# Performance work log

Hardware: AMD Instinct MI355X
Metric: run time of the kernel (lower is better)

Reference implementation:

```python
import jax, jax.numpy as jnp
import numpy as np

EMBED_DIM = 1024
NUM_HEADS = 16
HEAD_DIM = EMBED_DIM // NUM_HEADS
SCALE = HEAD_DIM ** (-0.5)


def setup_inputs() -> dict:
    key = jax.random.key(0)
    ks = jax.random.split(key, 8)
    B, Nq, Nkv, C = 2, 2048, 2048, EMBED_DIM
    s = C ** (-0.5)
    return {
        "q": jax.random.normal(ks[0], (B, Nq, C), dtype=jnp.float32),
        "kv": jax.random.normal(ks[1], (B, Nkv, C), dtype=jnp.float32),
        "w_q": jax.random.normal(ks[2], (C, C), dtype=jnp.float32) * s,
        "b_q": jnp.zeros((C,), dtype=jnp.float32),
        "w_kv": jax.random.normal(ks[3], (C, 2 * C), dtype=jnp.float32) * s,
        "b_kv": jnp.zeros((2 * C,), dtype=jnp.float32),
        "w_out": jax.random.normal(ks[4], (C, C), dtype=jnp.float32) * s,
        "b_out": jnp.zeros((C,), dtype=jnp.float32),
    }


def reference(q, kv, w_q, b_q, w_kv, b_kv, w_out, b_out):
    B, Nq, C = q.shape
    _, Nkv, _ = kv.shape
    H, D = NUM_HEADS, HEAD_DIM

    # q projection: (B, Nq, C) -> (B, H, Nq, D)
    qp = (q @ w_q + b_q).reshape(B, Nq, H, D).transpose(0, 2, 1, 3)

    # kv projection: (B, Nkv, 2C) -> (2, B, H, Nkv, D); '(two h d)' layout
    kvp = (kv @ w_kv + b_kv).reshape(B, Nkv, 2, H, D).transpose(2, 0, 3, 1, 4)
    kp, vp = kvp[0], kvp[1]

    # attention scores (B, H, Nq, Nkv), softmax over kv axis
    attn = jnp.einsum("bhqd,bhkd->bhqk", qp, kp) * SCALE
    attn = jax.nn.softmax(attn, axis=-1)

    out = jnp.einsum("bhqk,bhkd->bhqd", attn, vp)
    out = out.transpose(0, 2, 1, 3).reshape(B, Nq, C)
    return out @ w_out + b_out
```

## Files before the change

kernel.cpp:

```cpp
#include <hip/hip_runtime.h>

#define NUM_HEADS 16
#define HEAD_DIM 64
#define EMBED 1024

typedef __attribute__((ext_vector_type(8))) short short8;
typedef __attribute__((ext_vector_type(4))) short short4v;
typedef __attribute__((ext_vector_type(4))) float f32x4;

#if __has_builtin(__builtin_amdgcn_exp2f)
#define EXP2F(x) __builtin_amdgcn_exp2f(x)
#else
#define EXP2F(x) exp2f(x)
#endif

__device__ __forceinline__ f32x4 mfma16_bf16(short4v a, short4v b, f32x4 c) {
#if defined(__HIP_DEVICE_COMPILE__)
  return __builtin_amdgcn_mfma_f32_16x16x16bf16_1k(a, b, c, 0, 0, 0);
#else
  return c;
#endif
}

__device__ __forceinline__ unsigned pk_trunc(float x1, float x0) {
#if defined(__HIP_DEVICE_COMPILE__)
  return __builtin_amdgcn_perm(__builtin_bit_cast(unsigned, x1),
                               __builtin_bit_cast(unsigned, x0), 0x07060302u);
#else
  return 0;
#endif
}

__device__ __forceinline__ short f2bf(float f) {
  unsigned u = __builtin_bit_cast(unsigned, f);
  u += 0x7fffu + ((u >> 16) & 1u);
  return (short)(u >> 16);
}

__device__ __forceinline__ void gload_lds16(const void* g, void* l) {
  __builtin_amdgcn_global_load_lds(
      (const __attribute__((address_space(1))) void*)g,
      (__attribute__((address_space(3))) void*)l,
      16, 0, 0);
}

__device__ __forceinline__ void tr_body(const float* __restrict__ in,
                                        short* __restrict__ out, int R, int C,
                                        int bx, int by, float (*t)[33], int tid) {
  int tx = tid & 31, ty = tid >> 5;
#pragma unroll
  for (int i = 0; i < 32; i += 8)
    t[ty + i][tx] = in[(size_t)(by + ty + i) * C + bx + tx];
  __syncthreads();
#pragma unroll
  for (int i = 0; i < 32; i += 8)
    out[(size_t)(bx + ty + i) * R + by + tx] = f2bf(t[tx][ty + i]);
}

__global__ void prep(const float* __restrict__ w_q, short* __restrict__ wqt,
                     const float* __restrict__ w_kv, short* __restrict__ wkvt,
                     const float* __restrict__ w_out, short* __restrict__ wot,
                     const float* __restrict__ q, const float* __restrict__ kv,
                     short* __restrict__ qb, short* __restrict__ kvb) {
  __shared__ float t[32][33];
  int bid = blockIdx.x, tid = threadIdx.x;
  if (bid < 1024) {
    tr_body(w_q, wqt, 1024, 1024, (bid & 31) * 32, (bid >> 5) * 32, t, tid);
  } else if (bid < 3072) {
    int r = bid - 1024;
    tr_body(w_kv, wkvt, 1024, 2048, (r & 63) * 32, (r >> 6) * 32, t, tid);
  } else if (bid < 4096) {
    int r = bid - 3072;
    tr_body(w_out, wot, 1024, 1024, (r & 31) * 32, (r >> 5) * 32, t, tid);
  } else {
    int r = bid - 4096;
    const float* src = (r < 2048) ? q : kv;
    short* dst = (r < 2048) ? qb : kvb;
    size_t base = (size_t)(r & 2047) * 2048 + (size_t)tid * 8;
    f32x4 x = *(const f32x4*)(src + base);
    f32x4 y = *(const f32x4*)(src + base + 4);
    uint4 p = {pk_trunc(x[1], x[0]), pk_trunc(x[3], x[2]),
               pk_trunc(y[1], y[0]), pk_trunc(y[3], y[2])};
    *(uint4*)(dst + base) = p;
  }
}

template <int MODE>
__device__ __forceinline__ void gemm_body(short* As, short* Bs,
                                          const short* __restrict__ A,
                                          const short* __restrict__ Bt,
                                          const float* __restrict__ bias,
                                          void* __restrict__ Cptr, int N, int K,
                                          int m0, int n0, float scale) {
  const int tid = threadIdx.x;
  const int wave = tid >> 6, lane = tid & 63;
  const int quad = lane >> 4, l16 = lane & 15;
  const int wr = wave >> 1, wc = wave & 1;

  f32x4 acc[4][4];
#pragma unroll
  for (int i = 0; i < 4; i++)
#pragma unroll
    for (int j = 0; j < 4; j++) acc[i][j] = (f32x4)0.f;

  const int srow = lane >> 3;
  const int schk = (lane & 7) ^ (srow & 7);
  const int ABUF = 128 * 64;
  const int NT = K >> 6;

  auto stage = [&](int t, int slot) {
    int k0 = t * 64;
    short* Ad = As + slot * ABUF;
    short* Bd = Bs + slot * ABUF;
#pragma unroll
    for (int s = 0; s < 4; s++) {
      gload_lds16(A + (size_t)(m0 + s * 32 + wave * 8 + srow) * K + k0 + schk * 8,
                  Ad + s * 2048 + wave * 512);
      gload_lds16(Bt + (size_t)(n0 + s * 32 + wave * 8 + srow) * K + k0 + schk * 8,
                  Bd + s * 2048 + wave * 512);
    }
  };

  stage(0, 0);
  stage(1, 1);
  asm volatile("s_waitcnt vmcnt(8)" ::: "memory");
  __builtin_amdgcn_s_barrier();
  asm volatile("" ::: "memory");

  for (int t = 0; t < NT; ++t) {
    const short* Ac = As + (t & 1) * ABUF;
    const short* Bc = Bs + (t & 1) * ABUF;

    short8 a[4][2], b[4][2];
#pragma unroll
    for (int i = 0; i < 4; i++) {
      int row = wr * 64 + i * 16 + l16;
#pragma unroll
      for (int kh = 0; kh < 2; kh++) {
        int ch = (kh * 4 + quad) ^ (row & 7);
        a[i][kh] = *(const short8*)(Ac + row * 64 + ch * 8);
      }
    }
#pragma unroll
    for (int j = 0; j < 4; j++) {
      int row = wc * 64 + j * 16 + l16;
#pragma unroll
      for (int kh = 0; kh < 2; kh++) {
        int ch = (kh * 4 + quad) ^ (row & 7);
        b[j][kh] = *(const short8*)(Bc + row * 64 + ch * 8);
      }
    }
    asm volatile("s_waitcnt lgkmcnt(0)" ::: "memory");
    __builtin_amdgcn_sched_barrier(0);
    __builtin_amdgcn_s_barrier();
    asm volatile("" ::: "memory");

    if (t + 2 < NT) stage(t + 2, t & 1);

    __builtin_amdgcn_s_setprio(1);
#pragma unroll
    for (int i = 0; i < 4; i++)
#pragma unroll
      for (int j = 0; j < 4; j++) {
        acc[i][j] = __builtin_amdgcn_mfma_f32_16x16x32_bf16(a[i][0], b[j][0],
                                                            acc[i][j], 0, 0, 0);
        acc[i][j] = __builtin_amdgcn_mfma_f32_16x16x32_bf16(a[i][1], b[j][1],
                                                            acc[i][j], 0, 0, 0);
      }
    __builtin_amdgcn_s_setprio(0);
    asm volatile("" ::: "memory");

    if (t + 2 < NT) {
      asm volatile("s_waitcnt vmcnt(8)" ::: "memory");
      __builtin_amdgcn_s_barrier();
    } else if (t + 1 < NT) {
      asm volatile("s_waitcnt vmcnt(0)" ::: "memory");
      __builtin_amdgcn_s_barrier();
    }
    asm volatile("" ::: "memory");
  }

#pragma unroll
  for (int j = 0; j < 4; j++) {
    int col = n0 + wc * 64 + j * 16 + l16;
    float bv = bias[col];
    if (MODE == 2) {
      int vcol = col - 1024;
      int h = vcol >> 6, d = vcol & 63;
#pragma unroll
      for (int i = 0; i < 4; i++) {
        int rbase = m0 + wr * 64 + i * 16 + quad * 4;
        int b = rbase >> 11;
        int kvr = rbase & 2047;
        short pk[4];
#pragma unroll
        for (int r = 0; r < 4; r++) pk[r] = f2bf(acc[i][j][r] + bv);
        *(uint2*)((short*)Cptr + ((size_t)(b * 16 + h) * 64 + d) * 2048 + kvr) =
            *(uint2*)pk;
      }
    } else {
#pragma unroll
      for (int i = 0; i < 4; i++) {
        int rbase = m0 + wr * 64 + i * 16 + quad * 4;
#pragma unroll
        for (int r = 0; r < 4; r++) {
          float v = (acc[i][j][r] + bv) * scale;
          if (MODE == 1)
            ((float*)Cptr)[(size_t)(rbase + r) * N + col] = v;
          else
            ((short*)Cptr)[(size_t)(rbase + r) * N + col] = f2bf(v);
        }
      }
    }
  }
}

__global__ __launch_bounds__(256, 2)
void gemm_qkv(const short* __restrict__ qb, const short* __restrict__ kvb,
              const short* __restrict__ wqt, const short* __restrict__ wkvt,
              const float* __restrict__ b_q, const float* __restrict__ b_kv,
              short* __restrict__ qp, short* __restrict__ kvp,
              short* __restrict__ vt) {
  __shared__ short As[2 * 128 * 64];
  __shared__ short Bs[2 * 128 * 64];
  int y = blockIdx.y;
  int m0 = blockIdx.x * 128;
  if (y < 8) {
    gemm_body<0>(As, Bs, qb, wqt, b_q, qp, 1024, 1024, m0, y * 128, 0.125f);
  } else if (y < 16) {
    gemm_body<0>(As, Bs, kvb, wkvt, b_kv, kvp, 2048, 1024, m0, (y - 8) * 128, 1.f);
  } else {
    gemm_body<2>(As, Bs, kvb, wkvt, b_kv, vt, 2048, 1024, m0, (y - 8) * 128, 1.f);
  }
}

__global__ __launch_bounds__(256, 2)
void gemm_out(const short* __restrict__ A, const short* __restrict__ Bt,
              const float* __restrict__ bias, float* __restrict__ C) {
  __shared__ short As[2 * 128 * 64];
  __shared__ short Bs[2 * 128 * 64];
  gemm_body<1>(As, Bs, A, Bt, bias, C, 1024, 1024, blockIdx.x * 128,
               blockIdx.y * 128, 1.f);
}

__global__ __launch_bounds__(256)
void attn8(const short* __restrict__ qp, const short* __restrict__ kvp,
           const short* __restrict__ vt, short* __restrict__ aout,
           int B, int Nq, int Nkv) {
  __shared__ short Ks0[64 * 64], Ks1[64 * 64];
  __shared__ short Vs0[64 * 64], Vs1[64 * 64];

  const int tid = threadIdx.x;
  const int wave = tid >> 6, lane = tid & 63;
  const int quad = lane >> 4, l16 = lane & 15;

  const int wid = blockIdx.y * gridDim.x + blockIdx.x;
  const int sub = wid >> 3;
  const int bh = (wid & 7) * 4 + (sub >> 5);
  const int b = bh >> 4, h = bh & 15;
  const int q0 = (sub & 31) * 64;
  const int niter = Nkv / 64;

  const int qrow = q0 + wave * 16 + l16;
  const short* qbase = qp + ((size_t)b * Nq + qrow) * EMBED + h * HEAD_DIM;
  short8 aq0 = *(const short8*)(qbase + quad * 8);
  short8 aq1 = *(const short8*)(qbase + 32 + quad * 8);

  const int rl = lane >> 3;
  const int co = (lane & 7) ^ (rl & 7);
  const short* kgbase = kvp + (size_t)b * Nkv * 2048 + h * HEAD_DIM;
  const short* vgbase = vt + (size_t)(b * 16 + h) * 64 * 2048;

  f32x4 acc[4];
#pragma unroll
  for (int nt = 0; nt < 4; nt++) acc[nt] = (f32x4)0.f;
  float lsum = 0.f;

  const int swz_r = quad ^ (l16 & 7);
  const int swz_r4 = (quad + 4) ^ (l16 & 7);

  auto stage = [&](int it, short* Kd, short* Vd) {
    int kv0 = it * 64;
    gload_lds16(kgbase + (size_t)(kv0 + wave * 16 + rl) * 2048 + co * 8,
                Kd + wave * 1024);
    gload_lds16(kgbase + (size_t)(kv0 + wave * 16 + 8 + rl) * 2048 + co * 8,
                Kd + wave * 1024 + 512);
    gload_lds16(vgbase + (size_t)(wave * 16 + rl) * 2048 + kv0 + co * 8,
                Vd + wave * 1024);
    gload_lds16(vgbase + (size_t)(wave * 16 + 8 + rl) * 2048 + kv0 + co * 8,
                Vd + wave * 1024 + 512);
  };

  auto compute = [&](const short* Kt, const short* Vt_) {
    f32x4 s[4];
#pragma unroll
    for (int jt = 0; jt < 4; jt++) s[jt] = (f32x4)0.f;
    __builtin_amdgcn_s_setprio(1);
#pragma unroll
    for (int jt = 0; jt < 4; ++jt) {
      const short* kr = Kt + (jt * 16 + l16) * 64;
      short8 ka0 = *(const short8*)(kr + swz_r * 8);
      short8 ka1 = *(const short8*)(kr + swz_r4 * 8);
      s[jt] = __builtin_amdgcn_mfma_f32_16x16x32_bf16(ka0, aq0, s[jt], 0, 0, 0);
      s[jt] = __builtin_amdgcn_mfma_f32_16x16x32_bf16(ka1, aq1, s[jt], 0, 0, 0);
    }
    __builtin_amdgcn_s_setprio(0);
    short4v pf[4];
#pragma unroll
    for (int jt = 0; jt < 4; ++jt) {
      float e0 = EXP2F(__builtin_fmaf(s[jt][0], 1.44269504f, -17.3123405f));
      float e1 = EXP2F(__builtin_fmaf(s[jt][1], 1.44269504f, -17.3123405f));
      float e2 = EXP2F(__builtin_fmaf(s[jt][2], 1.44269504f, -17.3123405f));
      float e3 = EXP2F(__builtin_fmaf(s[jt][3], 1.44269504f, -17.3123405f));
      lsum += (e0 + e1) + (e2 + e3);
      uint2 pk = {pk_trunc(e1, e0), pk_trunc(e3, e2)};
      pf[jt] = __builtin_bit_cast(short4v, pk);
    }
    __builtin_amdgcn_s_setprio(1);
#pragma unroll
    for (int jt = 0; jt < 4; ++jt) {
      const int chs = ((jt * 2 + (quad >> 1)) ^ (l16 & 7)) * 8 + (quad & 1) * 4;
#pragma unroll
      for (int nt = 0; nt < 4; ++nt) {
        short4v va = *(const short4v*)(Vt_ + (nt * 16 + l16) * 64 + chs);
        acc[nt] = mfma16_bf16(va, pf[jt], acc[nt]);
      }
    }
    __builtin_amdgcn_s_setprio(0);
  };

  stage(0, Ks0, Vs0);
  for (int it = 0; it < niter; it += 2) {
    __syncthreads();
    stage(min(it + 1, niter - 1), Ks1, Vs1);
    compute(Ks0, Vs0);
    __syncthreads();
    stage(min(it + 2, niter - 1), Ks0, Vs0);
    compute(Ks1, Vs1);
  }

  lsum += __shfl_xor(lsum, 16);
  lsum += __shfl_xor(lsum, 32);
  float inv = 1.f / lsum;
  const int qg = q0 + wave * 16 + l16;
  short* obase = aout + ((size_t)b * Nq + qg) * EMBED + h * HEAD_DIM;
#pragma unroll
  for (int nt = 0; nt < 4; ++nt) {
    short pk[4];
#pragma unroll
    for (int r = 0; r < 4; ++r) pk[r] = f2bf(acc[nt][r] * inv);
    *(uint2*)(obase + nt * 16 + quad * 4) = *(uint2*)pk;
  }
}

extern "C" void kernel_launch(void* const* d_in, const int* in_sizes, int n_in,
                              void* d_out, int out_size, void* d_ws, size_t ws_size,
                              hipStream_t stream) {
  const float* q = (const float*)d_in[0];
  const float* kv = (const float*)d_in[1];
  const float* w_q = (const float*)d_in[2];
  const float* b_q = (const float*)d_in[3];
  const float* w_kv = (const float*)d_in[4];
  const float* b_kv = (const float*)d_in[5];
  const float* w_out = (const float*)d_in[6];
  const float* b_out = (const float*)d_in[7];

  const int B = 2, Nq = 2048, Nkv = 2048, C = 1024;
  const int Mq = B * Nq;

  char* ws = (char*)d_ws;
  short* qp = (short*)ws;
  short* kvp = qp + (size_t)Mq * C;
  short* vt = kvp + (size_t)Mq * 2 * C;
  short* aout = vt + (size_t)Mq * C;
  short* wot = aout + (size_t)Mq * C;
  short* wqt = wot + (size_t)C * C;
  short* wkvt = wqt + (size_t)C * C;
  short* qb = aout;
  short* kvb = (short*)d_out;

  prep<<<8192, 256, 0, stream>>>(w_q, wqt, w_kv, wkvt, w_out, wot, q, kv, qb, kvb);
  gemm_qkv<<<dim3(Mq / 128, 24), 256, 0, stream>>>(qb, kvb, wqt, wkvt, b_q, b_kv,
                                                   qp, kvp, vt);
  attn8<<<dim3(Nq / 64, B * NUM_HEADS), 256, 0, stream>>>(qp, kvp, vt, aout,
                                                          B, Nq, Nkv);
  gemm_out<<<dim3(Mq / 128, C / 128), 256, 0, stream>>>(aout, wot, b_out,
                                                        (float*)d_out);
}
```

Baseline: 202.2 us.

## Process 128 query rows per attention block, two 16-row tiles per wave

Each wave in the attention kernel now handles two 16-row query tiles instead of one, so a block covers 128 queries and the grid is halved. Every K and V tile staged into LDS and read into registers is reused across twice as many MFMAs, halving global K/V traffic and LDS reads per unit of work. In exchange, accumulator and score registers double, which may lower occupancy, and the grid drops to 512 blocks.

```diff
diff --git a/kernel.cpp b/kernel.cpp
--- a/kernel.cpp
+++ b/kernel.cpp
@@ -256,25 +256,32 @@
 
   const int wid = blockIdx.y * gridDim.x + blockIdx.x;
   const int sub = wid >> 3;
-  const int bh = (wid & 7) * 4 + (sub >> 5);
+  const int bh = (wid & 7) * 4 + (sub >> 4);
   const int b = bh >> 4, h = bh & 15;
-  const int q0 = (sub & 31) * 64;
+  const int q0 = (sub & 15) * 128;
   const int niter = Nkv / 64;
 
-  const int qrow = q0 + wave * 16 + l16;
-  const short* qbase = qp + ((size_t)b * Nq + qrow) * EMBED + h * HEAD_DIM;
-  short8 aq0 = *(const short8*)(qbase + quad * 8);
-  short8 aq1 = *(const short8*)(qbase + 32 + quad * 8);
+  short8 aq[2][2];
+#pragma unroll
+  for (int hh = 0; hh < 2; ++hh) {
+    const short* qbase =
+        qp + ((size_t)b * Nq + q0 + wave * 32 + hh * 16 + l16) * EMBED +
+        h * HEAD_DIM;
+    aq[hh][0] = *(const short8*)(qbase + quad * 8);
+    aq[hh][1] = *(const short8*)(qbase + 32 + quad * 8);
+  }
 
   const int rl = lane >> 3;
   const int co = (lane & 7) ^ (rl & 7);
   const short* kgbase = kvp + (size_t)b * Nkv * 2048 + h * HEAD_DIM;
   const short* vgbase = vt + (size_t)(b * 16 + h) * 64 * 2048;
 
-  f32x4 acc[4];
-#pragma unroll
-  for (int nt = 0; nt < 4; nt++) acc[nt] = (f32x4)0.f;
-  float lsum = 0.f;
+  f32x4 acc[2][4];
+#pragma unroll
+  for (int hh = 0; hh < 2; ++hh)
+#pragma unroll
+    for (int nt = 0; nt < 4; nt++) acc[hh][nt] = (f32x4)0.f;
+  float lsum0 = 0.f, lsum1 = 0.f;
 
   const int swz_r = quad ^ (l16 & 7);
   const int swz_r4 = (quad + 4) ^ (l16 & 7);
@@ -292,29 +299,44 @@
   };
 
   auto compute = [&](const short* Kt, const short* Vt_) {
-    f32x4 s[4];
-#pragma unroll
-    for (int jt = 0; jt < 4; jt++) s[jt] = (f32x4)0.f;
+    f32x4 s[2][4];
+#pragma unroll
+    for (int hh = 0; hh < 2; ++hh)
+#pragma unroll
+      for (int jt = 0; jt < 4; jt++) s[hh][jt] = (f32x4)0.f;
     __builtin_amdgcn_s_setprio(1);
 #pragma unroll
     for (int jt = 0; jt < 4; ++jt) {
       const short* kr = Kt + (jt * 16 + l16) * 64;
       short8 ka0 = *(const short8*)(kr + swz_r * 8);
       short8 ka1 = *(const short8*)(kr + swz_r4 * 8);
-      s[jt] = __builtin_amdgcn_mfma_f32_16x16x32_bf16(ka0, aq0, s[jt], 0, 0, 0);
-      s[jt] = __builtin_amdgcn_mfma_f32_16x16x32_bf16(ka1, aq1, s[jt], 0, 0, 0);
+      s[0][jt] = __builtin_amdgcn_mfma_f32_16x16x32_bf16(ka0, aq[0][0], s[0][jt], 0, 0, 0);
+      s[0][jt] = __builtin_amdgcn_mfma_f32_16x16x32_bf16(ka1, aq[0][1], s[0][jt], 0, 0, 0);
+      s[1][jt] = __builtin_amdgcn_mfma_f32_16x16x32_bf16(ka0, aq[1][0], s[1][jt], 0, 0, 0);
+      s[1][jt] = __builtin_amdgcn_mfma_f32_16x16x32_bf16(ka1, aq[1][1], s[1][jt], 0, 0, 0);
     }
     __builtin_amdgcn_s_setprio(0);
-    short4v pf[4];
+    short4v pf[2][4];
 #pragma unroll
     for (int jt = 0; jt < 4; ++jt) {
-      float e0 = EXP2F(__builtin_fmaf(s[jt][0], 1.44269504f, -17.3123405f));
-      float e1 = EXP2F(__builtin_fmaf(s[jt][1], 1.44269504f, -17.3123405f));
-      float e2 = EXP2F(__builtin_fmaf(s[jt][2], 1.44269504f, -17.3123405f));
-      float e3 = EXP2F(__builtin_fmaf(s[jt][3], 1.44269504f, -17.3123405f));
-      lsum += (e0 + e1) + (e2 + e3);
-      uint2 pk = {pk_trunc(e1, e0), pk_trunc(e3, e2)};
-      pf[jt] = __builtin_bit_cast(short4v, pk);
+      {
+        float e0 = EXP2F(__builtin_fmaf(s[0][jt][0], 1.44269504f, -17.3123405f));
+        float e1 = EXP2F(__builtin_fmaf(s[0][jt][1], 1.44269504f, -17.3123405f));
+        float e2 = EXP2F(__builtin_fmaf(s[0][jt][2], 1.44269504f, -17.3123405f));
+        float e3 = EXP2F(__builtin_fmaf(s[0][jt][3], 1.44269504f, -17.3123405f));
+        lsum0 += (e0 + e1) + (e2 + e3);
+        uint2 pk = {pk_trunc(e1, e0), pk_trunc(e3, e2)};
+        pf[0][jt] = __builtin_bit_cast(short4v, pk);
+      }
+      {
+        float e0 = EXP2F(__builtin_fmaf(s[1][jt][0], 1.44269504f, -17.3123405f));
+        float e1 = EXP2F(__builtin_fmaf(s[1][jt][1], 1.44269504f, -17.3123405f));
+        float e2 = EXP2F(__builtin_fmaf(s[1][jt][2], 1.44269504f, -17.3123405f));
+        float e3 = EXP2F(__builtin_fmaf(s[1][jt][3], 1.44269504f, -17.3123405f));
+        lsum1 += (e0 + e1) + (e2 + e3);
+        uint2 pk = {pk_trunc(e1, e0), pk_trunc(e3, e2)};
+        pf[1][jt] = __builtin_bit_cast(short4v, pk);
+      }
     }
     __builtin_amdgcn_s_setprio(1);
 #pragma unroll
@@ -323,7 +345,8 @@
 #pragma unroll
       for (int nt = 0; nt < 4; ++nt) {
         short4v va = *(const short4v*)(Vt_ + (nt * 16 + l16) * 64 + chs);
-        acc[nt] = mfma16_bf16(va, pf[jt], acc[nt]);
+        acc[0][nt] = mfma16_bf16(va, pf[0][jt], acc[0][nt]);
+        acc[1][nt] = mfma16_bf16(va, pf[1][jt], acc[1][nt]);
       }
     }
     __builtin_amdgcn_s_setprio(0);
@@ -339,17 +362,24 @@
     compute(Ks1, Vs1);
   }
 
-  lsum += __shfl_xor(lsum, 16);
-  lsum += __shfl_xor(lsum, 32);
-  float inv = 1.f / lsum;
-  const int qg = q0 + wave * 16 + l16;
-  short* obase = aout + ((size_t)b * Nq + qg) * EMBED + h * HEAD_DIM;
-#pragma unroll
-  for (int nt = 0; nt < 4; ++nt) {
-    short pk[4];
-#pragma unroll
-    for (int r = 0; r < 4; ++r) pk[r] = f2bf(acc[nt][r] * inv);
-    *(uint2*)(obase + nt * 16 + quad * 4) = *(uint2*)pk;
+  lsum0 += __shfl_xor(lsum0, 16);
+  lsum0 += __shfl_xor(lsum0, 32);
+  lsum1 += __shfl_xor(lsum1, 16);
+  lsum1 += __shfl_xor(lsum1, 32);
+  float inv0 = 1.f / lsum0;
+  float inv1 = 1.f / lsum1;
+#pragma unroll
+  for (int hh = 0; hh < 2; ++hh) {
+    float inv = hh ? inv1 : inv0;
+    const int qg = q0 + wave * 32 + hh * 16 + l16;
+    short* obase = aout + ((size_t)b * Nq + qg) * EMBED + h * HEAD_DIM;
+#pragma unroll
+    for (int nt = 0; nt < 4; ++nt) {
+      short pk[4];
+#pragma unroll
+      for (int r = 0; r < 4; ++r) pk[r] = f2bf(acc[hh][nt][r] * inv);
+      *(uint2*)(obase + nt * 16 + quad * 4) = *(uint2*)pk;
+    }
   }
 }
 
@@ -382,8 +412,8 @@
   prep<<<8192, 256, 0, stream>>>(w_q, wqt, w_kv, wkvt, w_out, wot, q, kv, qb, kvb);
   gemm_qkv<<<dim3(Mq / 128, 24), 256, 0, stream>>>(qb, kvb, wqt, wkvt, b_q, b_kv,
                                                    qp, kvp, vt);
-  attn8<<<dim3(Nq / 64, B * NUM_HEADS), 256, 0, stream>>>(qp, kvp, vt, aout,
-                                                          B, Nq, Nkv);
+  attn8<<<dim3(Nq / 128, B * NUM_HEADS), 256, 0, stream>>>(qp, kvp, vt, aout,
+                                                           B, Nq, Nkv);
   gemm_out<<<dim3(Mq / 128, C / 128), 256, 0, stream>>>(aout, wot, b_out,
                                                         (float*)d_out);
 }
```

After: 206.6 us. +2.1%, slower.

## Use permlane swaps to feed P into K=32 MFMAs and compute row sums via MFMA

Applied to the files above, without the earlier changes.

In the attention inner loop, the bf16 probability fragments are rearranged across lanes with permlane32/permlane16 swaps so the PV product can use 16x16x32 MFMAs with short8 V loads instead of 16x16x16 MFMAs. The softmax denominator is also accumulated by an extra MFMA against a vector of ones, replacing per-lane scalar adds and the final cross-lane shuffles. This halves the PV MFMA count and removes VALU sum work, at the cost of lane-permute instructions and one extra MFMA per 32 keys. The new path is only compiled when the permlane swap builtins exist (gfx950).

```diff
diff --git a/kernel.cpp b/kernel.cpp
--- a/kernel.cpp
+++ b/kernel.cpp
@@ -7,11 +7,17 @@
 typedef __attribute__((ext_vector_type(8))) short short8;
 typedef __attribute__((ext_vector_type(4))) short short4v;
 typedef __attribute__((ext_vector_type(4))) float f32x4;
+typedef __attribute__((ext_vector_type(2))) unsigned uint2v;
 
 #if __has_builtin(__builtin_amdgcn_exp2f)
 #define EXP2F(x) __builtin_amdgcn_exp2f(x)
 #else
 #define EXP2F(x) exp2f(x)
+#endif
+
+#if __has_builtin(__builtin_amdgcn_permlane32_swap) && \
+    __has_builtin(__builtin_amdgcn_permlane16_swap)
+#define HAVE_PLSWAP 1
 #endif
 
 __device__ __forceinline__ f32x4 mfma16_bf16(short4v a, short4v b, f32x4 c) {
@@ -274,7 +280,14 @@
   f32x4 acc[4];
 #pragma unroll
   for (int nt = 0; nt < 4; nt++) acc[nt] = (f32x4)0.f;
+#ifdef HAVE_PLSWAP
+  f32x4 lacc = (f32x4)0.f;
+  short8 ones;
+#pragma unroll
+  for (int i = 0; i < 8; ++i) ones[i] = (short)0x3F80;
+#else
   float lsum = 0.f;
+#endif
 
   const int swz_r = quad ^ (l16 & 7);
   const int swz_r4 = (quad + 4) ^ (l16 & 7);
@@ -305,6 +318,44 @@
       s[jt] = __builtin_amdgcn_mfma_f32_16x16x32_bf16(ka1, aq1, s[jt], 0, 0, 0);
     }
     __builtin_amdgcn_s_setprio(0);
+#ifdef HAVE_PLSWAP
+    unsigned pd0[4], pd1[4];
+#pragma unroll
+    for (int jt = 0; jt < 4; ++jt) {
+      float e0 = EXP2F(__builtin_fmaf(s[jt][0], 1.44269504f, -17.3123405f));
+      float e1 = EXP2F(__builtin_fmaf(s[jt][1], 1.44269504f, -17.3123405f));
+      float e2 = EXP2F(__builtin_fmaf(s[jt][2], 1.44269504f, -17.3123405f));
+      float e3 = EXP2F(__builtin_fmaf(s[jt][3], 1.44269504f, -17.3123405f));
+      pd0[jt] = pk_trunc(e1, e0);
+      pd1[jt] = pk_trunc(e3, e2);
+    }
+#pragma unroll
+    for (int j2 = 0; j2 < 2; ++j2) {
+      unsigned x0 = pd0[2 * j2], y0 = pd0[2 * j2 + 1];
+      unsigned x1 = pd1[2 * j2], y1 = pd1[2 * j2 + 1];
+      {
+        uint2v t = __builtin_amdgcn_permlane32_swap(x0, y0, false, false);
+        uint2v u = __builtin_amdgcn_permlane16_swap(t[0], t[1], false, false);
+        x0 = u[0]; y0 = u[1];
+      }
+      {
+        uint2v t = __builtin_amdgcn_permlane32_swap(x1, y1, false, false);
+        uint2v u = __builtin_amdgcn_permlane16_swap(t[0], t[1], false, false);
+        x1 = u[0]; y1 = u[1];
+      }
+      uint4 pbu = {x0, x1, y0, y1};
+      short8 pb = __builtin_bit_cast(short8, pbu);
+      __builtin_amdgcn_s_setprio(1);
+      lacc = __builtin_amdgcn_mfma_f32_16x16x32_bf16(ones, pb, lacc, 0, 0, 0);
+#pragma unroll
+      for (int nt = 0; nt < 4; ++nt) {
+        const int ch = ((j2 * 4 + quad) ^ (l16 & 7)) * 8;
+        short8 va = *(const short8*)(Vt_ + (nt * 16 + l16) * 64 + ch);
+        acc[nt] = __builtin_amdgcn_mfma_f32_16x16x32_bf16(va, pb, acc[nt], 0, 0, 0);
+      }
+      __builtin_amdgcn_s_setprio(0);
+    }
+#else
     short4v pf[4];
 #pragma unroll
     for (int jt = 0; jt < 4; ++jt) {
@@ -327,6 +378,7 @@
       }
     }
     __builtin_amdgcn_s_setprio(0);
+#endif
   };
 
   stage(0, Ks0, Vs0);
@@ -339,9 +391,13 @@
     compute(Ks1, Vs1);
   }
 
+#ifdef HAVE_PLSWAP
+  float inv = 1.f / lacc[0];
+#else
   lsum += __shfl_xor(lsum, 16);
   lsum += __shfl_xor(lsum, 32);
   float inv = 1.f / lsum;
+#endif
   const int qg = q0 + wave * 16 + l16;
   short* obase = aout + ((size_t)b * Nq + qg) * EMBED + h * HEAD_DIM;
 #pragma unroll
```

Measured after the change: 199.0 us. No clear change (-1.6%).
